# Optimization experiments

Hardware: AMD Instinct MI355X
Metric: run time of the kernel (lower is better)

## Reference

```python
import jax, jax.numpy as jnp
import numpy as np

D_MODEL = 1024
NHEAD = 16
HEAD_DIM = D_MODEL // NHEAD
MLP_DIM = 4096
ROPE_THETA = 10000.0


def layer_norm(x, g, b, eps=1e-5):
    mu = jnp.mean(x, axis=-1, keepdims=True)
    var = jnp.var(x, axis=-1, keepdims=True)
    return (x - mu) * jax.lax.rsqrt(var + eps) * g + b


def rope_cos_sin(seq_len, dim):
    # lucidrains RotaryEmbedding: inv_freq over even indices, freqs repeated interleaved
    inv_freq = 1.0 / (ROPE_THETA ** (jnp.arange(0, dim, 2, dtype=jnp.float32) / dim))
    t = jnp.arange(seq_len, dtype=jnp.float32)
    freqs = t[:, None] * inv_freq[None, :]            # (S, dim/2)
    freqs = jnp.repeat(freqs, 2, axis=-1)             # (S, dim) interleaved [f0,f0,f1,f1,...]
    return jnp.cos(freqs), jnp.sin(freqs)


def apply_rope(x, cos, sin):
    # x: (B, S, H, D); interleaved rotate_half: (x0,x1) -> (-x1, x0)
    x1 = x[..., ::2]
    x2 = x[..., 1::2]
    rot = jnp.stack([-x2, x1], axis=-1).reshape(x.shape)
    c = cos[None, :, None, :]
    s = sin[None, :, None, :]
    return x * c + rot * s


def setup_inputs() -> dict:
    key = jax.random.key(0)
    ks = jax.random.split(key, 8)
    B, S = 2, 2048
    sc = 1.0 / np.sqrt(D_MODEL)
    inputs = jax.random.normal(ks[0], (B, S, D_MODEL), dtype=jnp.float32)
    return {
        "inputs": inputs,
        "ln1_g": jnp.ones((D_MODEL,), jnp.float32),
        "ln1_b": jnp.zeros((D_MODEL,), jnp.float32),
        "Wq": jax.random.normal(ks[1], (D_MODEL, D_MODEL), jnp.float32) * sc,
        "Wk": jax.random.normal(ks[2], (D_MODEL, D_MODEL), jnp.float32) * sc,
        "Wv": jax.random.normal(ks[3], (D_MODEL, D_MODEL), jnp.float32) * sc,
        "Wo": jax.random.normal(ks[4], (D_MODEL, D_MODEL), jnp.float32) * sc,
        "ln2_g": jnp.ones((D_MODEL,), jnp.float32),
        "ln2_b": jnp.zeros((D_MODEL,), jnp.float32),
        "Wfc2": jax.random.normal(ks[5], (D_MODEL, MLP_DIM), jnp.float32) * sc,
        "bfc2": jnp.zeros((MLP_DIM,), jnp.float32),
        "Wfc3": jax.random.normal(ks[6], (MLP_DIM, D_MODEL), jnp.float32) * (1.0 / np.sqrt(MLP_DIM)),
        "bfc3": jnp.zeros((D_MODEL,), jnp.float32),
    }


def reference(inputs, ln1_g, ln1_b, Wq, Wk, Wv, Wo, ln2_g, ln2_b, Wfc2, bfc2, Wfc3, bfc3):
    B, S, _ = inputs.shape
    x = layer_norm(inputs, ln1_g, ln1_b)
    q = (x @ Wq).reshape(B, S, NHEAD, HEAD_DIM)
    k = (x @ Wk).reshape(B, S, NHEAD, HEAD_DIM)
    v = (x @ Wv).reshape(B, S, NHEAD, HEAD_DIM)
    cos, sin = rope_cos_sin(S, HEAD_DIM)
    q = apply_rope(q, cos, sin)
    k = apply_rope(k, cos, sin)
    scores = jnp.einsum('bqhd,bkhd->bhqk', q, k) / np.sqrt(HEAD_DIM)
    attn = jax.nn.softmax(scores, axis=-1)
    out = jnp.einsum('bhqk,bkhd->bqhd', attn, v).reshape(B, S, D_MODEL)
    out = out @ Wo
    mlp_in = out + inputs
    h = layer_norm(mlp_in, ln2_g, ln2_b)
    h = jax.nn.gelu(h @ Wfc2 + bfc2, approximate=False)
    h = h @ Wfc3 + bfc3
    return h + mlp_in
```

## Files before the change

### kernel.cpp

```cpp
#include <hip/hip_runtime.h>
#include <cstdint>
#include <cstddef>

typedef __bf16 bf16x8 __attribute__((ext_vector_type(8)));
typedef __bf16 bf16x4 __attribute__((ext_vector_type(4)));
typedef float  f32x4  __attribute__((ext_vector_type(4)));
typedef float  f32x16 __attribute__((ext_vector_type(16)));
typedef unsigned int u32x4 __attribute__((ext_vector_type(4)));

__device__ __forceinline__ void load16_to_lds(const void* g, void* l) {
  __builtin_amdgcn_global_load_lds(
      (const __attribute__((address_space(1))) void*)g,
      (__attribute__((address_space(3))) void*)l, 16, 0, 0);
}

__device__ __forceinline__ unsigned cvt_pk_bf16(float a, float b) {
  unsigned r;
  asm("v_cvt_pk_bf16_f32 %0, %1, %2" : "=v"(r) : "v"(a), "v"(b));
  return r;
}
__device__ __forceinline__ void permlane32_swap(unsigned &a, unsigned &b) {
  asm("v_permlane32_swap_b32 %0, %1" : "+v"(a), "+v"(b));
}

__global__ __launch_bounds__(256) void transpose_cast(
    const float* __restrict__ src, __bf16* __restrict__ dst, int K, int N)
{
  __shared__ float tile[32][33];
  const int n0 = blockIdx.x * 32, k0 = blockIdx.y * 32;
  const int tx = threadIdx.x, ty = threadIdx.y;
#pragma unroll
  for (int i = 0; i < 32; i += 8)
    tile[ty + i][tx] = src[(size_t)(k0 + ty + i) * N + n0 + tx];
  __syncthreads();
#pragma unroll
  for (int i = 0; i < 32; i += 8)
    dst[(size_t)(n0 + ty + i) * K + k0 + tx] = (__bf16)tile[tx][ty + i];
}

__global__ __launch_bounds__(256) void transpose_cast_qkv(
    const float* __restrict__ s0, const float* __restrict__ s1,
    const float* __restrict__ s2, __bf16* __restrict__ dst)
{
  __shared__ float tile[32][33];
  const float* src = blockIdx.z == 0 ? s0 : blockIdx.z == 1 ? s1 : s2;
  __bf16* d = dst + (size_t)blockIdx.z * 1024 * 1024;
  const int n0 = blockIdx.x * 32, k0 = blockIdx.y * 32;
  const int tx = threadIdx.x, ty = threadIdx.y;
#pragma unroll
  for (int i = 0; i < 32; i += 8)
    tile[ty + i][tx] = src[(size_t)(k0 + ty + i) * 1024 + n0 + tx];
  __syncthreads();
#pragma unroll
  for (int i = 0; i < 32; i += 8)
    d[(size_t)(n0 + ty + i) * 1024 + k0 + tx] = (__bf16)tile[tx][ty + i];
}

__global__ __launch_bounds__(256) void ln_kernel(
    const float* __restrict__ x, const float* __restrict__ g,
    const float* __restrict__ bta, __bf16* __restrict__ out)
{
  const int row = blockIdx.x;
  const int t = threadIdx.x;
  const float4 v = ((const float4*)(x + (size_t)row * 1024))[t];
  float s  = v.x + v.y + v.z + v.w;
  float ss = v.x * v.x + v.y * v.y + v.z * v.z + v.w * v.w;
#pragma unroll
  for (int o = 32; o > 0; o >>= 1) { s += __shfl_down(s, o); ss += __shfl_down(ss, o); }
  __shared__ float rs[4], rss[4];
  const int w = t >> 6, l = t & 63;
  if (l == 0) { rs[w] = s; rss[w] = ss; }
  __syncthreads();
  s  = rs[0] + rs[1] + rs[2] + rs[3];
  ss = rss[0] + rss[1] + rss[2] + rss[3];
  const float mu = s * (1.0f / 1024.0f);
  const float var = ss * (1.0f / 1024.0f) - mu * mu;
  const float rstd = rsqrtf(var + 1e-5f);
  const float4 gg = ((const float4*)g)[t];
  const float4 bb = ((const float4*)bta)[t];
  __bf16* o = out + (size_t)row * 1024 + t * 4;
  o[0] = (__bf16)((v.x - mu) * rstd * gg.x + bb.x);
  o[1] = (__bf16)((v.y - mu) * rstd * gg.y + bb.y);
  o[2] = (__bf16)((v.z - mu) * rstd * gg.z + bb.z);
  o[3] = (__bf16)((v.w - mu) * rstd * gg.w + bb.w);
}

enum { EPI_BF16 = 0, EPI_RES_F32 = 1, EPI_GELU_BF16 = 2, EPI_BIAS_RES_F32 = 3 };

template <int TM, int KB, int EPI>
__global__ __launch_bounds__(256, 2) void gemm_bf16(
    const __bf16* __restrict__ A, const __bf16* __restrict__ Bt,
    __bf16* __restrict__ outb, float* __restrict__ outf,
    const float* __restrict__ bias, const float* __restrict__ res,
    int M, int N, int K)
{
  constexpr int MT = TM / 32;
  constexpr int KS = KB / 32;
  __shared__ __bf16 As0[TM * KB], As1[TM * KB];
  __shared__ __bf16 Bs0[128 * KB], Bs1[128 * KB];
  const int tid  = threadIdx.x;
  const int lane = tid & 63, w = tid >> 6;
  const int wm = w >> 1, wn = w & 1;
  const int quad = lane >> 4, l16 = lane & 15;
  const int m0 = blockIdx.y * TM, n0 = blockIdx.x * 128;

  f32x4 acc[MT][4] = {};
  const __bf16* Ag = A  + (size_t)m0 * K;
  const __bf16* Bg = Bt + (size_t)n0 * K;

#define G_STAGE(AsX, BsX, k0) {                                            \
    _Pragma("unroll")                                                      \
    for (int r2 = 0; r2 < TM * KB / 2048; ++r2) {                          \
      const int c = r2 * 256 + tid;                                        \
      const int r = c / (KB / 8), cb = c % (KB / 8);                       \
      const int g = (KB == 64) ? (cb ^ (r & 7)) : cb;                      \
      load16_to_lds(Ag + (size_t)r * K + (k0) + g * 8, &AsX[c * 8]);       \
    }                                                                      \
    _Pragma("unroll")                                                      \
    for (int r2 = 0; r2 < KB / 16; ++r2) {                                 \
      const int c = r2 * 256 + tid;                                        \
      const int r = c / (KB / 8), cb = c % (KB / 8);                       \
      const int g = (KB == 64) ? (cb ^ (r & 7)) : cb;                      \
      load16_to_lds(Bg + (size_t)r * K + (k0) + g * 8, &BsX[c * 8]);       \
    } }

#define G_COMPUTE(AsX, BsX) {                                              \
    bf16x8 af[MT][KS], bfr[4][KS];                                         \
    _Pragma("unroll")                                                      \
    for (int mt = 0; mt < MT; ++mt) {                                      \
      const int row = wm * (TM / 2) + mt * 16 + l16;                       \
      _Pragma("unroll")                                                    \
      for (int ks = 0; ks < KS; ++ks) {                                    \
        const int ch = (KB == 64) ? ((ks * 4 + quad) ^ (row & 7)) : quad;  \
        af[mt][ks] = *(const bf16x8*)&AsX[row * KB + ch * 8];              \
      }                                                                    \
    }                                                                      \
    _Pragma("unroll")                                                      \
    for (int nt = 0; nt < 4; ++nt) {                                       \
      const int row = wn * 64 + nt * 16 + l16;                             \
      _Pragma("unroll")                                                    \
      for (int ks = 0; ks < KS; ++ks) {                                    \
        const int ch = (KB == 64) ? ((ks * 4 + quad) ^ (row & 7)) : quad;  \
        bfr[nt][ks] = *(const bf16x8*)&BsX[row * KB + ch * 8];             \
      }                                                                    \
    }                                                                      \
    _Pragma("unroll")                                                      \
    for (int ks = 0; ks < KS; ++ks)                                        \
      _Pragma("unroll")                                                    \
      for (int mt = 0; mt < MT; ++mt)                                      \
        _Pragma("unroll")                                                  \
        for (int nt = 0; nt < 4; ++nt)                                     \
          acc[mt][nt] = __builtin_amdgcn_mfma_f32_16x16x32_bf16(           \
              af[mt][ks], bfr[nt][ks], acc[mt][nt], 0, 0, 0);              \
  }

  G_STAGE(As0, Bs0, 0);
  const int nk = K / KB;
  for (int kt = 0; kt < nk; kt += 2) {
    __syncthreads();
    if (kt + 1 < nk) G_STAGE(As1, Bs1, (kt + 1) * KB);
    G_COMPUTE(As0, Bs0);
    __syncthreads();
    if (kt + 2 < nk) G_STAGE(As0, Bs0, (kt + 2) * KB);
    G_COMPUTE(As1, Bs1);
  }
#undef G_STAGE
#undef G_COMPUTE

#pragma unroll
  for (int mt = 0; mt < MT; ++mt) {
#pragma unroll
    for (int nt = 0; nt < 4; ++nt) {
      const int col = n0 + wn * 64 + nt * 16 + l16;
#pragma unroll
      for (int i = 0; i < 4; ++i) {
        const int row = m0 + wm * (TM / 2) + mt * 16 + quad * 4 + i;
        float v = acc[mt][nt][i];
        const size_t idx = (size_t)row * N + col;
        if (EPI == EPI_BF16) {
          outb[idx] = (__bf16)v;
        } else if (EPI == EPI_RES_F32) {
          outf[idx] = v + res[idx];
        } else if (EPI == EPI_GELU_BF16) {
          v += bias[col];
          outb[idx] = (__bf16)(0.5f * v * (1.0f + erff(v * 0.70710678118f)));
        } else {
          v += bias[col];
          outf[idx] = v + res[idx];
        }
      }
    }
  }
}

__global__ __launch_bounds__(256) void rope_qk(
    const __bf16* __restrict__ qkv, __bf16* __restrict__ qr, __bf16* __restrict__ kr)
{
  const int idx = blockIdx.x * 256 + threadIdx.x;
  const int d2 = idx & 31;
  const int h  = (idx >> 5) & 15;
  const int bs = idx >> 9;
  const int s  = bs & 2047;
  const int b  = bs >> 11;
  const float inv_freq = exp2f(-((float)d2 * (1.0f / 32.0f)) * 13.2877123795f);
  const float ang = (float)s * inv_freq;
  const float c = cosf(ang), sn = sinf(ang);
  const float QS = 0.125f * 1.44269504f;
  const __bf16* qp = qkv + (size_t)bs * 3072 + h * 64 + 2 * d2;
  const __bf16* kp = qp + 1024;
  const float q0 = (float)qp[0], q1 = (float)qp[1];
  const float k0 = (float)kp[0], k1 = (float)kp[1];
  const size_t o = ((size_t)(b * 16 + h) * 2048 + s) * 64 + 2 * d2;
  qr[o]     = (__bf16)((q0 * c - q1 * sn) * QS);
  qr[o + 1] = (__bf16)((q1 * c + q0 * sn) * QS);
  kr[o]     = (__bf16)(k0 * c - k1 * sn);
  kr[o + 1] = (__bf16)(k1 * c + k0 * sn);
}

__global__ __launch_bounds__(256) void v_transpose(
    const __bf16* __restrict__ qkv, __bf16* __restrict__ vt)
{
  __shared__ __bf16 t[64][72];
  const int st = blockIdx.x, h = blockIdx.y, b = blockIdx.z;
  const int tx = threadIdx.x & 63, ty = threadIdx.x >> 6;
  const int s0 = st * 64;
  const __bf16* src = qkv + ((size_t)(b * 2048 + s0)) * 3072 + 2048 + h * 64;
#pragma unroll
  for (int i = 0; i < 64; i += 4)
    t[ty + i][tx] = src[(size_t)(ty + i) * 3072 + tx];
  __syncthreads();
  __bf16* dst = vt + ((size_t)(b * 16 + h) * 64) * 2048 + s0;
#pragma unroll
  for (int i = 0; i < 64; i += 4)
    dst[(size_t)(ty + i) * 2048 + tx] = t[tx][ty + i];
}

__global__ __launch_bounds__(256, 2) void attn_kernel(
    const __bf16* __restrict__ qr, const __bf16* __restrict__ kr,
    const __bf16* __restrict__ vt, __bf16* __restrict__ attn_o)
{
  constexpr int S = 2048, DH = 64, NH = 16, BQ = 128, BKK = 64;
  __shared__ __align__(16) __bf16 Qs[BQ * 64];
  __shared__ __align__(16) __bf16 Ks0[64 * 64], Ks1[64 * 64];
  __shared__ __align__(16) __bf16 Vts0[64 * 64], Vts1[64 * 64];

  const int tid = threadIdx.x;
  const int lane = tid & 63, w = tid >> 6;
  const int l32 = lane & 31, half = lane >> 5;
  const int qt = blockIdx.x, h = blockIdx.y, b = blockIdx.z;
  const int bh = b * NH + h;
  const __bf16* Q  = qr + ((size_t)bh * S + qt * BQ) * DH;
  const __bf16* Kp = kr + (size_t)bh * S * DH;
  const __bf16* Vp = vt + (size_t)bh * DH * S;
  __bf16* Pb = Qs + w * 2048;

#define A_STAGE(KsX, VtsX, kk) {                                           \
    _Pragma("unroll")                                                      \
    for (int r2 = 0; r2 < 2; ++r2) {                                       \
      const int c = r2 * 256 + tid;                                        \
      const int r = c >> 3, cb = c & 7;                                    \
      const int cg = (cb ^ (r & 7)) * 8;                                   \
      load16_to_lds(Kp + (size_t)((kk) + r) * DH + cg, &KsX[c * 8]);       \
      load16_to_lds(Vp + (size_t)r * S + (kk) + cg, &VtsX[c * 8]);         \
    } }

#pragma unroll
  for (int r4 = 0; r4 < 4; ++r4) {
    const int c = r4 * 256 + tid;
    const int r = c >> 3, cb = c & 7;
    load16_to_lds(Q + (size_t)r * DH + ((cb ^ (r & 7)) * 8), &Qs[c * 8]);
  }
  A_STAGE(Ks0, Vts0, 0);
  __syncthreads();

  bf16x8 qfB[4];
  {
    const int row = w * 32 + l32;
#pragma unroll
    for (int c = 0; c < 4; ++c)
      qfB[c] = *(const bf16x8*)&Qs[row * 64 + (((2 * c + half) ^ (row & 7)) * 8)];
  }

  float mreg = -3.0e38f, lreg = 0.0f;
  f32x16 oacc[2] = {};

#define A_COMPUTE(KsX, VtsX) {                                             \
    bf16x8 kf[2][4], vf[2][4];                                             \
    _Pragma("unroll")                                                      \
    for (int t = 0; t < 2; ++t) {                                          \
      const int row = 32 * t + l32;                                        \
      _Pragma("unroll")                                                    \
      for (int c = 0; c < 4; ++c)                                          \
        kf[t][c] = *(const bf16x8*)&KsX[row * 64 + (((2 * c + half) ^ (l32 & 7)) * 8)]; \
    }                                                                      \
    _Pragma("unroll")                                                      \
    for (int v = 0; v < 2; ++v) {                                          \
      const int row = 32 * v + l32;                                        \
      _Pragma("unroll")                                                    \
      for (int c = 0; c < 4; ++c)                                          \
        vf[v][c] = *(const bf16x8*)&VtsX[row * 64 + (((2 * c + half) ^ (l32 & 7)) * 8)]; \
    }                                                                      \
    f32x16 sa[2] = {};                                                     \
    __builtin_amdgcn_s_setprio(1);                                         \
    _Pragma("unroll")                                                      \
    for (int t = 0; t < 2; ++t)                                            \
      _Pragma("unroll")                                                    \
      for (int c = 0; c < 4; ++c)                                          \
        sa[t] = __builtin_amdgcn_mfma_f32_32x32x16_bf16(kf[t][c], qfB[c], sa[t], 0, 0, 0); \
    __builtin_amdgcn_s_setprio(0);                                         \
    float pm[8];                                                           \
    _Pragma("unroll")                                                      \
    for (int t = 0; t < 2; ++t)                                            \
      _Pragma("unroll")                                                    \
      for (int g = 0; g < 4; ++g)                                          \
        pm[t * 4 + g] = fmaxf(fmaxf(sa[t][4 * g], sa[t][4 * g + 1]),       \
                              fmaxf(sa[t][4 * g + 2], sa[t][4 * g + 3]));  \
    float mx = fmaxf(fmaxf(fmaxf(pm[0], pm[1]), fmaxf(pm[2], pm[3])),      \
                     fmaxf(fmaxf(pm[4], pm[5]), fmaxf(pm[6], pm[7])));     \
    mx = fmaxf(mx, __shfl_xor(mx, 32));                                    \
    float mnew = mreg;                                                     \
    if (!__all(mx <= mreg + 8.0f)) {                                       \
      mnew = fmaxf(mreg, mx);                                              \
      const float alpha = __builtin_amdgcn_exp2f(mreg - mnew);             \
      mreg = mnew;                                                         \
      lreg *= alpha;                                                       \
      _Pragma("unroll")                                                    \
      for (int v = 0; v < 2; ++v)                                          \
        _Pragma("unroll")                                                  \
        for (int r = 0; r < 16; ++r) oacc[v][r] *= alpha;                  \
    }                                                                      \
    float ps0 = 0.f, ps1 = 0.f, ps2 = 0.f, ps3 = 0.f;                      \
    _Pragma("unroll")                                                      \
    for (int t = 0; t < 2; ++t)                                            \
      _Pragma("unroll")                                                    \
      for (int r = 0; r < 16; r += 4) {                                    \
        const float p0 = __builtin_amdgcn_exp2f(sa[t][r]     - mnew);      \
        const float p1 = __builtin_amdgcn_exp2f(sa[t][r + 1] - mnew);      \
        const float p2 = __builtin_amdgcn_exp2f(sa[t][r + 2] - mnew);      \
        const float p3 = __builtin_amdgcn_exp2f(sa[t][r + 3] - mnew);      \
        sa[t][r] = p0; sa[t][r + 1] = p1;                                  \
        sa[t][r + 2] = p2; sa[t][r + 3] = p3;                              \
        ps0 += p0; ps1 += p1; ps2 += p2; ps3 += p3;                        \
      }                                                                    \
    float sum = (ps0 + ps1) + (ps2 + ps3);                                 \
    sum += __shfl_xor(sum, 32);                                            \
    lreg += sum;                                                           \
    __builtin_amdgcn_s_setprio(1);                                         \
    _Pragma("unroll")                                                      \
    for (int c = 0; c < 4; ++c) {                                          \
      const int t = c >> 1, r0 = (c & 1) * 8;                              \
      unsigned px = cvt_pk_bf16(sa[t][r0],     sa[t][r0 + 1]);             \
      unsigned py = cvt_pk_bf16(sa[t][r0 + 2], sa[t][r0 + 3]);             \
      unsigned pz = cvt_pk_bf16(sa[t][r0 + 4], sa[t][r0 + 5]);             \
      unsigned pw = cvt_pk_bf16(sa[t][r0 + 6], sa[t][r0 + 7]);             \
      permlane32_swap(px, pz);                                             \
      permlane32_swap(py, pw);                                             \
      const u32x4 pv4 = { px, py, pz, pw };                                \
      const bf16x8 pf = __builtin_bit_cast(bf16x8, pv4);                   \
      oacc[0] = __builtin_amdgcn_mfma_f32_32x32x16_bf16(vf[0][c], pf, oacc[0], 0, 0, 0); \
      oacc[1] = __builtin_amdgcn_mfma_f32_32x32x16_bf16(vf[1][c], pf, oacc[1], 0, 0, 0); \
    }                                                                      \
    __builtin_amdgcn_s_setprio(0);                                         \
  }

  for (int kt = 0; kt < S / BKK; kt += 2) {
    __syncthreads();
    if (kt + 1 < S / BKK) A_STAGE(Ks1, Vts1, (kt + 1) * BKK);
    A_COMPUTE(Ks0, Vts0);
    __syncthreads();
    if (kt + 2 < S / BKK) A_STAGE(Ks0, Vts0, (kt + 2) * BKK);
    A_COMPUTE(Ks1, Vts1);
  }
#undef A_STAGE
#undef A_COMPUTE

  const float linv = 1.0f / lreg;
#pragma unroll
  for (int v = 0; v < 2; ++v)
#pragma unroll
    for (int g = 0; g < 4; ++g) {
      bf16x4 ov;
#pragma unroll
      for (int i = 0; i < 4; ++i) ov[i] = (__bf16)(oacc[v][4 * g + i] * linv);
      const int dc = 4 * v + g;
      *(bf16x4*)&Pb[l32 * 64 + ((dc ^ (l32 & 7)) * 8) + 4 * half] = ov;
    }
#pragma unroll
  for (int cc = 0; cc < 4; ++cc) {
    const int c = cc * 64 + lane;
    const int r = c >> 3, g = c & 7;
    const bf16x8 od = *(const bf16x8*)&Pb[r * 64 + ((g ^ (r & 7)) * 8)];
    const int srow = qt * BQ + w * 32 + r;
    *(bf16x8*)&attn_o[((size_t)b * S + srow) * 1024 + h * 64 + g * 8] = od;
  }
}

extern "C" void kernel_launch(void* const* d_in, const int* in_sizes, int n_in,
                              void* d_out, int out_size, void* d_ws, size_t ws_size,
                              hipStream_t stream) {
  const float* inputs = (const float*)d_in[0];
  const float* ln1_g  = (const float*)d_in[1];
  const float* ln1_b  = (const float*)d_in[2];
  const float* Wq     = (const float*)d_in[3];
  const float* Wk     = (const float*)d_in[4];
  const float* Wv     = (const float*)d_in[5];
  const float* Wo     = (const float*)d_in[6];
  const float* ln2_g  = (const float*)d_in[7];
  const float* ln2_b  = (const float*)d_in[8];
  const float* Wfc2   = (const float*)d_in[9];
  const float* bfc2   = (const float*)d_in[10];
  const float* Wfc3   = (const float*)d_in[11];
  const float* bfc3   = (const float*)d_in[12];
  float* out = (float*)d_out;
  char* ws = (char*)d_ws;
  const size_t MB = 1024 * 1024;

  __bf16* Wqkv_t = (__bf16*)(ws);
  __bf16* Wo_t   = (__bf16*)(ws + 6 * MB);
  __bf16* Wfc2_t = (__bf16*)(ws + 8 * MB);
  __bf16* Wfc3_t = (__bf16*)(ws + 16 * MB);
  __bf16* xb     = (__bf16*)(ws + 24 * MB);
  __bf16* attn_o = xb;
  __bf16* qkv    = (__bf16*)(ws + 32 * MB);
  float*  mlp_in = (float*)(ws + 32 * MB);
  __bf16* h2     = (__bf16*)(ws + 48 * MB);
  __bf16* qrb    = (__bf16*)(ws + 56 * MB);
  __bf16* krb    = (__bf16*)(ws + 64 * MB);
  __bf16* vtb    = (__bf16*)(ws + 72 * MB);
  __bf16* hbuf   = (__bf16*)(ws + 56 * MB);

  const dim3 tb(32, 8);
  transpose_cast_qkv<<<dim3(32, 32, 3), tb, 0, stream>>>(Wq, Wk, Wv, Wqkv_t);
  transpose_cast<<<dim3(32, 32),  tb, 0, stream>>>(Wo,   Wo_t,   1024, 1024);
  transpose_cast<<<dim3(128, 32), tb, 0, stream>>>(Wfc2, Wfc2_t, 1024, 4096);
  transpose_cast<<<dim3(32, 128), tb, 0, stream>>>(Wfc3, Wfc3_t, 4096, 1024);

  ln_kernel<<<4096, 256, 0, stream>>>(inputs, ln1_g, ln1_b, xb);

  gemm_bf16<128, 32, EPI_BF16><<<dim3(24, 32), 256, 0, stream>>>(
      xb, Wqkv_t, qkv, nullptr, nullptr, nullptr, 4096, 3072, 1024);

  rope_qk<<<8192, 256, 0, stream>>>(qkv, qrb, krb);
  v_transpose<<<dim3(32, 16, 2), 256, 0, stream>>>(qkv, vtb);

  attn_kernel<<<dim3(16, 16, 2), 256, 0, stream>>>(qrb, krb, vtb, attn_o);

  gemm_bf16<64, 64, EPI_RES_F32><<<dim3(8, 64), 256, 0, stream>>>(
      attn_o, Wo_t, nullptr, mlp_in, nullptr, inputs, 4096, 1024, 1024);

  ln_kernel<<<4096, 256, 0, stream>>>(mlp_in, ln2_g, ln2_b, h2);

  gemm_bf16<128, 32, EPI_GELU_BF16><<<dim3(32, 32), 256, 0, stream>>>(
      h2, Wfc2_t, hbuf, nullptr, bfc2, nullptr, 4096, 4096, 1024);

  gemm_bf16<64, 64, EPI_BIAS_RES_F32><<<dim3(8, 64), 256, 0, stream>>>(
      hbuf, Wfc3_t, nullptr, out, bfc3, mlp_in, 4096, 1024, 4096);
}
```

Before: 343.7 us.

## Software-pipeline attention: overlap next-tile QK MFMA with current softmax·V, 4-stage buffering

Splits the attention inner step into a QK score stage and a softmax+PV stage, and issues the QK MFMAs for tile k+1 before the softmax/PV work of tile k, using two score register sets. K/V LDS buffering grows from two to four stages, so loads are issued two tiles ahead. The aim is to hide exp/max/convert latency behind matrix-core work and to hide more of the global load latency. In exchange it uses more registers (32 extra accumulator VGPRs) and twice the LDS, which may lower occupancy below the 2-blocks-per-CU launch bound.

```diff
diff --git a/kernel.cpp b/kernel.cpp
--- a/kernel.cpp
+++ b/kernel.cpp
@@ -241,8 +241,8 @@
 {
   constexpr int S = 2048, DH = 64, NH = 16, BQ = 128, BKK = 64;
   __shared__ __align__(16) __bf16 Qs[BQ * 64];
-  __shared__ __align__(16) __bf16 Ks0[64 * 64], Ks1[64 * 64];
-  __shared__ __align__(16) __bf16 Vts0[64 * 64], Vts1[64 * 64];
+  __shared__ __align__(16) __bf16 Ks0[64 * 64], Ks1[64 * 64], Ks2[64 * 64], Ks3[64 * 64];
+  __shared__ __align__(16) __bf16 Vts0[64 * 64], Vts1[64 * 64], Vts2[64 * 64], Vts3[64 * 64];
 
   const int tid = threadIdx.x;
   const int lane = tid & 63, w = tid >> 6;
@@ -271,6 +271,7 @@
     load16_to_lds(Q + (size_t)r * DH + ((cb ^ (r & 7)) * 8), &Qs[c * 8]);
   }
   A_STAGE(Ks0, Vts0, 0);
+  A_STAGE(Ks1, Vts1, BKK);
   __syncthreads();
 
   bf16x8 qfB[4];
@@ -283,9 +284,11 @@
 
   float mreg = -3.0e38f, lreg = 0.0f;
   f32x16 oacc[2] = {};
-
-#define A_COMPUTE(KsX, VtsX) {                                             \
-    bf16x8 kf[2][4], vf[2][4];                                             \
+  const f32x16 zz = {};
+  f32x16 saA[2], saB[2];
+
+#define A_QK(KsX, saX) {                                                   \
+    bf16x8 kf[2][4];                                                       \
     _Pragma("unroll")                                                      \
     for (int t = 0; t < 2; ++t) {                                          \
       const int row = 32 * t + l32;                                        \
@@ -293,6 +296,19 @@
       for (int c = 0; c < 4; ++c)                                          \
         kf[t][c] = *(const bf16x8*)&KsX[row * 64 + (((2 * c + half) ^ (l32 & 7)) * 8)]; \
     }                                                                      \
+    __builtin_amdgcn_s_setprio(1);                                         \
+    _Pragma("unroll")                                                      \
+    for (int t = 0; t < 2; ++t) {                                          \
+      saX[t] = __builtin_amdgcn_mfma_f32_32x32x16_bf16(kf[t][0], qfB[0], zz, 0, 0, 0); \
+      _Pragma("unroll")                                                    \
+      for (int c = 1; c < 4; ++c)                                          \
+        saX[t] = __builtin_amdgcn_mfma_f32_32x32x16_bf16(kf[t][c], qfB[c], saX[t], 0, 0, 0); \
+    }                                                                      \
+    __builtin_amdgcn_s_setprio(0);                                         \
+  }
+
+#define A_SMPV(saC, VtsX) {                                                \
+    bf16x8 vf[2][4];                                                       \
     _Pragma("unroll")                                                      \
     for (int v = 0; v < 2; ++v) {                                          \
       const int row = 32 * v + l32;                                        \
@@ -300,21 +316,13 @@
       for (int c = 0; c < 4; ++c)                                          \
         vf[v][c] = *(const bf16x8*)&VtsX[row * 64 + (((2 * c + half) ^ (l32 & 7)) * 8)]; \
     }                                                                      \
-    f32x16 sa[2] = {};                                                     \
-    __builtin_amdgcn_s_setprio(1);                                         \
+    float pm[8];                                                           \
     _Pragma("unroll")                                                      \
     for (int t = 0; t < 2; ++t)                                            \
       _Pragma("unroll")                                                    \
-      for (int c = 0; c < 4; ++c)                                          \
-        sa[t] = __builtin_amdgcn_mfma_f32_32x32x16_bf16(kf[t][c], qfB[c], sa[t], 0, 0, 0); \
-    __builtin_amdgcn_s_setprio(0);                                         \
-    float pm[8];                                                           \
-    _Pragma("unroll")                                                      \
-    for (int t = 0; t < 2; ++t)                                            \
-      _Pragma("unroll")                                                    \
       for (int g = 0; g < 4; ++g)                                          \
-        pm[t * 4 + g] = fmaxf(fmaxf(sa[t][4 * g], sa[t][4 * g + 1]),       \
-                              fmaxf(sa[t][4 * g + 2], sa[t][4 * g + 3]));  \
+        pm[t * 4 + g] = fmaxf(fmaxf(saC[t][4 * g], saC[t][4 * g + 1]),     \
+                              fmaxf(saC[t][4 * g + 2], saC[t][4 * g + 3]));\
     float mx = fmaxf(fmaxf(fmaxf(pm[0], pm[1]), fmaxf(pm[2], pm[3])),      \
                      fmaxf(fmaxf(pm[4], pm[5]), fmaxf(pm[6], pm[7])));     \
     mx = fmaxf(mx, __shfl_xor(mx, 32));                                    \
@@ -334,25 +342,22 @@
     for (int t = 0; t < 2; ++t)                                            \
       _Pragma("unroll")                                                    \
       for (int r = 0; r < 16; r += 4) {                                    \
-        const float p0 = __builtin_amdgcn_exp2f(sa[t][r]     - mnew);      \
-        const float p1 = __builtin_amdgcn_exp2f(sa[t][r + 1] - mnew);      \
-        const float p2 = __builtin_amdgcn_exp2f(sa[t][r + 2] - mnew);      \
-        const float p3 = __builtin_amdgcn_exp2f(sa[t][r + 3] - mnew);      \
-        sa[t][r] = p0; sa[t][r + 1] = p1;                                  \
-        sa[t][r + 2] = p2; sa[t][r + 3] = p3;                              \
+        const float p0 = __builtin_amdgcn_exp2f(saC[t][r]     - mnew);     \
+        const float p1 = __builtin_amdgcn_exp2f(saC[t][r + 1] - mnew);     \
+        const float p2 = __builtin_amdgcn_exp2f(saC[t][r + 2] - mnew);     \
+        const float p3 = __builtin_amdgcn_exp2f(saC[t][r + 3] - mnew);     \
+        saC[t][r] = p0; saC[t][r + 1] = p1;                                \
+        saC[t][r + 2] = p2; saC[t][r + 3] = p3;                            \
         ps0 += p0; ps1 += p1; ps2 += p2; ps3 += p3;                        \
       }                                                                    \
-    float sum = (ps0 + ps1) + (ps2 + ps3);                                 \
-    sum += __shfl_xor(sum, 32);                                            \
-    lreg += sum;                                                           \
     __builtin_amdgcn_s_setprio(1);                                         \
     _Pragma("unroll")                                                      \
     for (int c = 0; c < 4; ++c) {                                          \
       const int t = c >> 1, r0 = (c & 1) * 8;                              \
-      unsigned px = cvt_pk_bf16(sa[t][r0],     sa[t][r0 + 1]);             \
-      unsigned py = cvt_pk_bf16(sa[t][r0 + 2], sa[t][r0 + 3]);             \
-      unsigned pz = cvt_pk_bf16(sa[t][r0 + 4], sa[t][r0 + 5]);             \
-      unsigned pw = cvt_pk_bf16(sa[t][r0 + 6], sa[t][r0 + 7]);             \
+      unsigned px = cvt_pk_bf16(saC[t][r0],     saC[t][r0 + 1]);           \
+      unsigned py = cvt_pk_bf16(saC[t][r0 + 2], saC[t][r0 + 3]);           \
+      unsigned pz = cvt_pk_bf16(saC[t][r0 + 4], saC[t][r0 + 5]);           \
+      unsigned pw = cvt_pk_bf16(saC[t][r0 + 6], saC[t][r0 + 7]);           \
       permlane32_swap(px, pz);                                             \
       permlane32_swap(py, pw);                                             \
       const u32x4 pv4 = { px, py, pz, pw };                                \
@@ -361,18 +366,34 @@
       oacc[1] = __builtin_amdgcn_mfma_f32_32x32x16_bf16(vf[1][c], pf, oacc[1], 0, 0, 0); \
     }                                                                      \
     __builtin_amdgcn_s_setprio(0);                                         \
-  }
-
-  for (int kt = 0; kt < S / BKK; kt += 2) {
-    __syncthreads();
-    if (kt + 1 < S / BKK) A_STAGE(Ks1, Vts1, (kt + 1) * BKK);
-    A_COMPUTE(Ks0, Vts0);
-    __syncthreads();
-    if (kt + 2 < S / BKK) A_STAGE(Ks0, Vts0, (kt + 2) * BKK);
-    A_COMPUTE(Ks1, Vts1);
-  }
+    float sum = (ps0 + ps1) + (ps2 + ps3);                                 \
+    sum += __shfl_xor(sum, 32);                                            \
+    lreg += sum;                                                           \
+  }
+
+#define A_PHASE(KsNext, VtsCur, KsSt, VtsSt, saCur, saNext, kkSt, DO_QK, DO_ST) { \
+    __syncthreads();                                                       \
+    if (DO_ST) A_STAGE(KsSt, VtsSt, kkSt);                                 \
+    if (DO_QK) A_QK(KsNext, saNext);                                       \
+    A_SMPV(saCur, VtsCur);                                                 \
+  }
+
+  A_QK(Ks0, saA);
+
+  for (int p = 0; p < 28; p += 4) {
+    A_PHASE(Ks1, Vts0, Ks2, Vts2, saA, saB, (p + 2) * BKK, true, true);
+    A_PHASE(Ks2, Vts1, Ks3, Vts3, saB, saA, (p + 3) * BKK, true, true);
+    A_PHASE(Ks3, Vts2, Ks0, Vts0, saA, saB, (p + 4) * BKK, true, true);
+    A_PHASE(Ks0, Vts3, Ks1, Vts1, saB, saA, (p + 5) * BKK, true, true);
+  }
+  A_PHASE(Ks1, Vts0, Ks2, Vts2, saA, saB, 30 * BKK, true, true);
+  A_PHASE(Ks2, Vts1, Ks3, Vts3, saB, saA, 31 * BKK, true, true);
+  A_PHASE(Ks3, Vts2, Ks0, Vts0, saA, saB, 0,        true, false);
+  A_PHASE(Ks0, Vts3, Ks1, Vts1, saB, saA, 0,        false, false);
 #undef A_STAGE
-#undef A_COMPUTE
+#undef A_QK
+#undef A_SMPV
+#undef A_PHASE
 
   const float linv = 1.0f / lreg;
 #pragma unroll
```

Result: no change. 345.0 us, median of 2 (+0.4%).
